# Kernel optimization log

Measured on AMD Instinct MI355X. Metric: run time of the kernel, lower is better.

The kernel has to match this reference:

```python
import jax, jax.numpy as jnp
import numpy as np

H = 512; W = 512; C = 32; B = 2; N = 120000; HEADS = 2; HD = C // HEADS; S = 9
INDEX_SHIFT = jnp.array([[0,0],[-1,0],[1,0],[0,1],[-1,1],[1,1],[0,-1],[-1,-1],[1,-1]], dtype=jnp.int32)


def setup_inputs() -> dict:
    key = jax.random.key(0)
    ks = jax.random.split(key, 20)
    bev_feats = jax.random.normal(ks[0], (B, N, C), jnp.float32)
    coors = []
    for b in range(B):
        perm = jax.random.permutation(ks[1 + b], H * W)[:N]
        coors.append(jnp.stack([perm // W, perm % W], axis=-1))
    bev_coors = jnp.stack(coors).astype(jnp.int32)
    s = 1.0 / np.sqrt(C)
    u = lambda k, shape, lim: jax.random.uniform(k, shape, jnp.float32, -lim, lim)
    return {
        'bev_feats': bev_feats,
        'bev_coors': bev_coors,
        'ln_w': jnp.ones((C,), jnp.float32),
        'ln_b': jnp.zeros((C,), jnp.float32),
        'wq': u(ks[3], (C, C), s), 'bq': u(ks[4], (C,), s),
        'wk': u(ks[5], (C, C), s), 'bk': u(ks[6], (C,), s),
        'wv': u(ks[7], (C, C), s), 'bv': u(ks[8], (C,), s),
        'pos_w': u(ks[9], (C, 2), 1.0 / np.sqrt(2.0)), 'pos_b': u(ks[10], (C,), 1.0 / np.sqrt(2.0)),
        'in_w': u(ks[11], (3 * C, C), s), 'in_b': jnp.zeros((3 * C,), jnp.float32),
        'out_w': u(ks[12], (C, C), s), 'out_b': jnp.zeros((C,), jnp.float32),
    }


def reference(bev_feats, bev_coors, ln_w, ln_b, wq, bq, wk, bk, wv, bv, pos_w, pos_b, in_w, in_b, out_w, out_b):
    def single(feats, coors):
        # LayerNorm (biased var, eps=1e-5)
        mu = feats.mean(-1, keepdims=True)
        var = feats.var(-1, keepdims=True)
        x = (feats - mu) / jnp.sqrt(var + 1e-5) * ln_w + ln_b
        # qkv 1x1 conv == linear
        q = x @ wq.T + bq
        k = x @ wk.T + bk
        v = x @ wv.T + bv
        # dense grid lookup: coord -> voxel index (-1 if empty)
        flat0 = coors[:, 0] * W + coors[:, 1]
        grid = jnp.full((H * W,), -1, jnp.int32).at[flat0].set(jnp.arange(N, dtype=jnp.int32))
        sc = coors[None] + INDEX_SHIFT[:, None]                      # [9,N,2]
        valid = (sc[..., 0] >= 0) & (sc[..., 0] < H) & (sc[..., 1] >= 0) & (sc[..., 1] < W)
        flat = jnp.clip(sc[..., 0], 0, H - 1) * W + jnp.clip(sc[..., 1], 0, W - 1)
        idx = jnp.where(valid, grid[flat], -1)                       # [9,N]
        pos = INDEX_SHIFT.astype(x.dtype) @ pos_w.T + pos_b          # [9,C]
        m = (idx >= 0)[..., None]
        tv = jnp.where(m, v[idx] + pos[:, None, :], 0.0)             # [9,N,C]
        tk = jnp.where(m, k[idx], 0.0)
        keyt = jnp.swapaxes(tk, 0, 1)                                # [N,9,C]
        valt = jnp.swapaxes(tv, 0, 1)
        # tiny MHA: query len 1, kv len 9, 2 heads (dropout inactive at eval)
        qp = q @ in_w[:C].T + in_b[:C]
        kp = keyt @ in_w[C:2 * C].T + in_b[C:2 * C]
        vp = valt @ in_w[2 * C:].T + in_b[2 * C:]
        qh = qp.reshape(N, HEADS, HD)
        kh = kp.reshape(N, S, HEADS, HD)
        vh = vp.reshape(N, S, HEADS, HD)
        attn = jax.nn.softmax(jnp.einsum('nhd,nshd->nhs', qh, kh) / np.sqrt(HD), axis=-1)
        o = jnp.einsum('nhs,nshd->nhd', attn, vh).reshape(N, C)
        o = o @ out_w.T + out_b
        # scatter to pseudo image [C,H,W]
        canvas = jnp.zeros((C, H * W), o.dtype).at[:, flat0].set(o.T)
        return canvas.reshape(C, H, W)
    return jax.vmap(single)(bev_feats, bev_coors)
```

## Files before the change

### kernel.cpp

```cpp
#include <hip/hip_runtime.h>
#include <hip/hip_fp16.h>
#include <cstdio>
#include <cstdint>

#define HH 512
#define WW 512
#define CC 32
#define BB 2
#define NN 120000
#define HWPIX (HH*WW)
#define NPTS (BB*NN)
#define NPIX (BB*HWPIX)
#define NBLK (NPIX/256)

__device__ __forceinline__ void h8_to_f8(float4 raw, float* o) {
    const __half2* h = (const __half2*)&raw;
    #pragma unroll
    for (int i = 0; i < 4; ++i) {
        float2 f = __half22float2(h[i]);
        o[2 * i] = f.x; o[2 * i + 1] = f.y;
    }
}

__global__ __launch_bounds__(256) void prep(const float* __restrict__ wq, const float* __restrict__ wk,
                          const float* __restrict__ wv, const float* __restrict__ in_w,
                          const float* __restrict__ out_w,
                          const float* __restrict__ bq, const float* __restrict__ bk,
                          const float* __restrict__ bv, const float* __restrict__ in_b,
                          const float* __restrict__ pos_w, const float* __restrict__ pos_b,
                          float* __restrict__ M, float* __restrict__ V, int* __restrict__ fmap_i) {
    int blk = blockIdx.x;
    if (blk < 16) {
        int tid = blk * 256 + threadIdx.x;
        int which = tid >> 10;
        int e = tid & 1023;
        int cp = e & 31;
        int j  = e >> 5;
        if (which < 3) {
            const float* w = (which == 0) ? wq : ((which == 1) ? wk : wv);
            const float* Wrow = in_w + (which * 32 + cp) * 32;
            float acc = 0.f;
            #pragma unroll
            for (int t = 0; t < 32; ++t) acc += Wrow[t] * w[t * 32 + j];
            M[which * 1024 + j * 32 + cp] = acc;
        } else {
            M[3 * 1024 + j * 32 + cp] = out_w[cp * 32 + j];
        }
    } else if (blk == 16) {
        int tid = threadIdx.x;
        if (tid < 32) {
            float a = 0.f, b = 0.f, c = 0.f;
            #pragma unroll
            for (int t = 0; t < 32; ++t) {
                a += in_w[tid * 32 + t] * bq[t];
                b += in_w[(32 + tid) * 32 + t] * bk[t];
                c += in_w[(64 + tid) * 32 + t] * bv[t];
            }
            V[tid]      = a + in_b[tid];
            V[32 + tid] = b;
            V[64 + tid] = c;
        } else if (tid < 128) {
            int grp = (tid - 32) >> 5;
            int cp  = tid & 31;
            float acc = 0.f;
            #pragma unroll
            for (int t = 0; t < 32; ++t) {
                float src = (grp == 0) ? pos_w[t * 2 + 0] : ((grp == 1) ? pos_w[t * 2 + 1] : pos_b[t]);
                acc += in_w[(64 + cp) * 32 + t] * src;
            }
            V[96 + grp * 32 + cp] = acc;
        }
    } else {
        int base = (blk - 17) * 2048 + threadIdx.x * 8;
        int4 z = {0, 0, 0, 0};
        *(int4*)(fmap_i + base)     = z;
        *(int4*)(fmap_i + base + 4) = z;
    }
}

__global__ __launch_bounds__(256) void stage1(const float* __restrict__ feats,
                                              const int* __restrict__ coors,
                                              const float* __restrict__ ln_w,
                                              const float* __restrict__ ln_b,
                                              const float* __restrict__ M,
                                              const float* __restrict__ V,
                                              __half* __restrict__ qh,
                                              __half* __restrict__ kvh,
                                              unsigned char* __restrict__ fmap) {
    int gp = blockIdx.x * 256 + threadIdx.x;
    if (gp >= NPTS) return;
    int b = (gp >= NN) ? 1 : 0;
    int2 yx = ((const int2*)coors)[gp];
    int pix = (b << 18) + (yx.x << 9) + yx.y;

    const float* fr = feats + ((size_t)gp << 5);
    float x[32];
    #pragma unroll
    for (int k = 0; k < 8; ++k) ((float4*)x)[k] = ((const float4*)fr)[k];

    float s1 = 0.f, s2 = 0.f;
    #pragma unroll
    for (int j = 0; j < 32; ++j) { s1 += x[j]; s2 += x[j] * x[j]; }
    float mu   = s1 * (1.f / 32.f);
    float var  = s2 * (1.f / 32.f) - mu * mu;
    float rstd = rsqrtf(var + 1e-5f);
    #pragma unroll
    for (int j = 0; j < 32; ++j) x[j] = (x[j] - mu) * rstd * ln_w[j] + ln_b[j];

    float acc[32];
    __half2 hbuf[16];

    #pragma unroll
    for (int c = 0; c < 32; ++c) acc[c] = V[c];
    #pragma unroll
    for (int j = 0; j < 32; ++j) {
        float xv = x[j];
        #pragma unroll
        for (int c = 0; c < 32; ++c) acc[c] += xv * M[j * 32 + c];
    }
    #pragma unroll
    for (int c = 0; c < 16; ++c) hbuf[c] = __floats2half2_rn(acc[2 * c], acc[2 * c + 1]);
    {
        float4* qd = (float4*)(qh + ((size_t)pix << 5));
        #pragma unroll
        for (int k = 0; k < 4; ++k) qd[k] = ((float4*)hbuf)[k];
    }

    __half2 kvbuf[32];

    #pragma unroll
    for (int c = 0; c < 32; ++c) acc[c] = V[32 + c];
    #pragma unroll
    for (int j = 0; j < 32; ++j) {
        float xv = x[j];
        #pragma unroll
        for (int c = 0; c < 32; ++c) acc[c] += xv * M[1024 + j * 32 + c];
    }
    #pragma unroll
    for (int c = 0; c < 16; ++c) kvbuf[c] = __floats2half2_rn(acc[2 * c], acc[2 * c + 1]);

    #pragma unroll
    for (int c = 0; c < 32; ++c) acc[c] = V[64 + c];
    #pragma unroll
    for (int j = 0; j < 32; ++j) {
        float xv = x[j];
        #pragma unroll
        for (int c = 0; c < 32; ++c) acc[c] += xv * M[2048 + j * 32 + c];
    }
    #pragma unroll
    for (int c = 0; c < 16; ++c) kvbuf[16 + c] = __floats2half2_rn(acc[2 * c], acc[2 * c + 1]);

    float4* kd = (float4*)(kvh + ((size_t)pix << 6));
    #pragma unroll
    for (int k = 0; k < 8; ++k) kd[k] = ((float4*)kvbuf)[k];

    fmap[pix] = 1;
}

__global__ __launch_bounds__(256) void stage23(const unsigned char* __restrict__ fmap,
                                               const __half* __restrict__ qh,
                                               const __half* __restrict__ kvh,
                                               const float* __restrict__ M,
                                               const float* __restrict__ V,
                                               const float* __restrict__ in_b,
                                               const float* __restrict__ out_b,
                                               float* __restrict__ out) {
    __shared__ __half2 lso[256 * 17];
    __shared__ int lsp[256];
    __shared__ int woff[4];

    int w = (blockIdx.x & 7) * 256 + (blockIdx.x >> 3);
    int tid = threadIdx.x;
    int pix = w * 256 + tid;

    bool occ = fmap[pix] != 0;
    unsigned long long mask = __ballot(occ);
    int lane = tid & 63, wvi = tid >> 6;
    if (lane == 0) woff[wvi] = __popcll(mask);
    __syncthreads();
    int pre = 0;
    for (int ww = 0; ww < wvi; ++ww) pre += woff[ww];
    int cnt = woff[0] + woff[1] + woff[2] + woff[3];
    int slot = -1;
    if (occ) {
        slot = pre + __popcll(mask & ((1ull << lane) - 1ull));
        lsp[slot] = tid;
    }
    __syncthreads();

    const int DYC[9] = {0,-1,1,0,-1,1,0,-1,1};
    const int DXC[9] = {0,0,0,1,1,1,-1,-1,-1};

    if (tid < cnt) {
        int pixl = w * 256 + lsp[tid];
        int b = pixl >> 18;
        int p = pixl & (HWPIX - 1);
        int y = p >> 9, x = p & 511;

        float qf[32];
        {
            const float4* q4 = (const float4*)(qh + ((size_t)pixl << 5));
            float4 r0 = q4[0], r1 = q4[1], r2 = q4[2], r3 = q4[3];
            h8_to_f8(r0, qf); h8_to_f8(r1, qf + 8); h8_to_f8(r2, qf + 16); h8_to_f8(r3, qf + 24);
        }

        int np[9];
        bool nv[9];
        #pragma unroll
        for (int s = 0; s < 9; ++s) {
            int sy = y + DYC[s], sx = x + DXC[s];
            bool inb = (sy >= 0) & (sy < HH) & (sx >= 0) & (sx < WW);
            int npx = (b << 18) + (sy << 9) + sx;
            np[s] = npx;
            nv[s] = inb ? (fmap[npx] != 0) : false;
        }

        float eb0 = 0.f, eb1 = 0.f;
        #pragma unroll
        for (int c = 0; c < 16; ++c) {
            eb0 += qf[c]      * in_b[32 + c];
            eb1 += qf[16 + c] * in_b[48 + c];
        }

        float lg0[9], lg1[9];
        #pragma unroll
        for (int s = 0; s < 9; ++s) {
            float d0 = eb0, d1 = eb1;
            if (nv[s]) {
                const float4* kp = (const float4*)(kvh + ((size_t)np[s] << 6));
                float kf[32];
                h8_to_f8(kp[0], kf);      h8_to_f8(kp[1], kf + 8);
                h8_to_f8(kp[2], kf + 16); h8_to_f8(kp[3], kf + 24);
                #pragma unroll
                for (int c = 0; c < 16; ++c) {
                    d0 += qf[c]      * kf[c];
                    d1 += qf[16 + c] * kf[16 + c];
                }
            }
            lg0[s] = d0 * 0.25f;
            lg1[s] = d1 * 0.25f;
        }
        float m0 = lg0[0], m1 = lg1[0];
        #pragma unroll
        for (int s = 1; s < 9; ++s) { m0 = fmaxf(m0, lg0[s]); m1 = fmaxf(m1, lg1[s]); }
        float l0 = 0.f, l1 = 0.f;
        #pragma unroll
        for (int s = 0; s < 9; ++s) {
            lg0[s] = __expf(lg0[s] - m0); l0 += lg0[s];
            lg1[s] = __expf(lg1[s] - m1); l1 += lg1[s];
        }

        float o[32];
        #pragma unroll
        for (int c = 0; c < 32; ++c) o[c] = 0.f;
        float wdy0 = 0.f, wdx0 = 0.f, woc0 = 0.f;
        float wdy1 = 0.f, wdx1 = 0.f, woc1 = 0.f;
        #pragma unroll
        for (int s = 0; s < 9; ++s) {
            if (nv[s]) {
                float w0 = lg0[s], w1 = lg1[s];
                const float4* vp = (const float4*)(kvh + ((size_t)np[s] << 6)) + 4;
                float vf[32];
                h8_to_f8(vp[0], vf);      h8_to_f8(vp[1], vf + 8);
                h8_to_f8(vp[2], vf + 16); h8_to_f8(vp[3], vf + 24);
                #pragma unroll
                for (int c = 0; c < 16; ++c) {
                    o[c]      += w0 * vf[c];
                    o[16 + c] += w1 * vf[16 + c];
                }
                wdy0 += w0 * (float)DYC[s]; wdx0 += w0 * (float)DXC[s]; woc0 += w0;
                wdy1 += w1 * (float)DYC[s]; wdx1 += w1 * (float)DXC[s]; woc1 += w1;
            }
        }
        float rl0 = 1.f / l0, rl1 = 1.f / l1;
        #pragma unroll
        for (int c = 0; c < 16; ++c) {
            o[c]      = (o[c]      + wdy0 * V[96 + c]      + wdx0 * V[128 + c]      + woc0 * V[160 + c])      * rl0 + in_b[64 + c];
            o[16 + c] = (o[16 + c] + wdy1 * V[96 + 16 + c] + wdx1 * V[128 + 16 + c] + woc1 * V[160 + 16 + c]) * rl1 + in_b[80 + c];
        }

        float acc[32];
        #pragma unroll
        for (int c = 0; c < 32; ++c) acc[c] = out_b[c];
        #pragma unroll
        for (int j = 0; j < 32; ++j) {
            float vj = o[j];
            #pragma unroll
            for (int c = 0; c < 32; ++c) acc[c] += vj * M[3072 + j * 32 + c];
        }

        __half2* lrow = lso + tid * 17;
        #pragma unroll
        for (int c = 0; c < 16; ++c) lrow[c] = __floats2half2_rn(acc[2 * c], acc[2 * c + 1]);
    }
    __syncthreads();

    int b = pix >> 18;
    int p = pix & (HWPIX - 1);
    float* outb = out + (size_t)b * CC * HWPIX + p;
    if (occ) {
        const __half2* lrow = lso + slot * 17;
        #pragma unroll
        for (int c2 = 0; c2 < 16; ++c2) {
            float2 f = __half22float2(lrow[c2]);
            outb[(2 * c2) * HWPIX]     = f.x;
            outb[(2 * c2 + 1) * HWPIX] = f.y;
        }
    } else {
        #pragma unroll
        for (int cc = 0; cc < 32; ++cc) outb[cc * HWPIX] = 0.f;
    }
}

extern "C" void kernel_launch(void* const* d_in, const int* in_sizes, int n_in,
                              void* d_out, int out_size, void* d_ws, size_t ws_size,
                              hipStream_t stream) {
    const float* feats = (const float*)d_in[0];
    const int*   coors = (const int*)d_in[1];
    const float* ln_w  = (const float*)d_in[2];
    const float* ln_b  = (const float*)d_in[3];
    const float* wq    = (const float*)d_in[4];
    const float* bq    = (const float*)d_in[5];
    const float* wk    = (const float*)d_in[6];
    const float* bk    = (const float*)d_in[7];
    const float* wv    = (const float*)d_in[8];
    const float* bv    = (const float*)d_in[9];
    const float* pos_w = (const float*)d_in[10];
    const float* pos_b = (const float*)d_in[11];
    const float* in_w  = (const float*)d_in[12];
    const float* in_b  = (const float*)d_in[13];
    const float* out_w = (const float*)d_in[14];
    const float* out_b = (const float*)d_in[15];

    float*  M    = (float*)d_ws;
    float*  V    = M + 4096;
    __half* qh   = (__half*)(V + 192);
    __half* kvh  = qh + (size_t)NPIX * 32;
    unsigned char* fmap = (unsigned char*)(kvh + (size_t)NPIX * 64);
    size_t need = (4096 + 192) * 4 + (size_t)NPIX * 96 * 2 + (size_t)NPIX;
    if (ws_size < need) {
        fprintf(stderr, "kernel_launch: ws too small: %zu < %zu\n", ws_size, need);
        return;
    }

    prep<<<81, 256, 0, stream>>>(wq, wk, wv, in_w, out_w, bq, bk, bv, in_b, pos_w, pos_b,
                                 M, V, (int*)fmap);
    stage1<<<(NPTS + 255) / 256, 256, 0, stream>>>(feats, coors, ln_w, ln_b, M, V, qh, kvh, fmap);
    stage23<<<NBLK, 256, 0, stream>>>(fmap, qh, kvh, M, V, in_b, out_b, (float*)d_out);
}
```

Measured before the change: 193.3 us.

## Split per-pixel attention across two threads, one per head

Each occupied pixel is now processed by two adjacent threads, each handling one attention head's key/value gathers, softmax and weighted sum. Head outputs are exchanged via a lane shuffle before the output projection, and each thread writes half of the output channels to shared memory. This raises lane utilization of the compacted work and lowers per-thread register pressure. In exchange, the output projection is computed redundantly in both threads.

```diff
diff --git a/kernel.cpp b/kernel.cpp
--- a/kernel.cpp
+++ b/kernel.cpp
@@ -165,7 +165,7 @@
                                                const float* __restrict__ in_b,
                                                const float* __restrict__ out_b,
                                                float* __restrict__ out) {
-    __shared__ __half2 lso[256 * 17];
+    __shared__ __half2 lso[256 * 18];
     __shared__ int lsp[256];
     __shared__ int woff[4];
 
@@ -191,17 +191,18 @@
     const int DYC[9] = {0,-1,1,0,-1,1,0,-1,1};
     const int DXC[9] = {0,0,0,1,1,1,-1,-1,-1};
 
-    if (tid < cnt) {
-        int pixl = w * 256 + lsp[tid];
+    for (int task = tid; task < 2 * cnt; task += 256) {
+        int i = task >> 1, h = task & 1;
+        int pixl = w * 256 + lsp[i];
         int b = pixl >> 18;
         int p = pixl & (HWPIX - 1);
         int y = p >> 9, x = p & 511;
 
-        float qf[32];
+        float qf[16];
         {
-            const float4* q4 = (const float4*)(qh + ((size_t)pixl << 5));
-            float4 r0 = q4[0], r1 = q4[1], r2 = q4[2], r3 = q4[3];
-            h8_to_f8(r0, qf); h8_to_f8(r1, qf + 8); h8_to_f8(r2, qf + 16); h8_to_f8(r3, qf + 24);
+            const float4* q4 = (const float4*)(qh + ((size_t)pixl << 5) + (h << 4));
+            float4 r0 = q4[0], r1 = q4[1];
+            h8_to_f8(r0, qf); h8_to_f8(r1, qf + 8);
         }
 
         int np[9];
@@ -215,68 +216,68 @@
             nv[s] = inb ? (fmap[npx] != 0) : false;
         }
 
-        float eb0 = 0.f, eb1 = 0.f;
-        #pragma unroll
-        for (int c = 0; c < 16; ++c) {
-            eb0 += qf[c]      * in_b[32 + c];
-            eb1 += qf[16 + c] * in_b[48 + c];
-        }
-
-        float lg0[9], lg1[9];
+        float eb = 0.f;
+        {
+            const float* ib = in_b + 32 + (h << 4);
+            #pragma unroll
+            for (int c = 0; c < 16; ++c) eb += qf[c] * ib[c];
+        }
+
+        float lg[9];
         #pragma unroll
         for (int s = 0; s < 9; ++s) {
-            float d0 = eb0, d1 = eb1;
+            float d = eb;
             if (nv[s]) {
-                const float4* kp = (const float4*)(kvh + ((size_t)np[s] << 6));
-                float kf[32];
-                h8_to_f8(kp[0], kf);      h8_to_f8(kp[1], kf + 8);
-                h8_to_f8(kp[2], kf + 16); h8_to_f8(kp[3], kf + 24);
+                const float4* kp = (const float4*)(kvh + ((size_t)np[s] << 6) + (h << 4));
+                float kf[16];
+                float4 k0 = kp[0], k1 = kp[1];
+                h8_to_f8(k0, kf); h8_to_f8(k1, kf + 8);
                 #pragma unroll
-                for (int c = 0; c < 16; ++c) {
-                    d0 += qf[c]      * kf[c];
-                    d1 += qf[16 + c] * kf[16 + c];
-                }
+                for (int c = 0; c < 16; ++c) d += qf[c] * kf[c];
             }
-            lg0[s] = d0 * 0.25f;
-            lg1[s] = d1 * 0.25f;
-        }
-        float m0 = lg0[0], m1 = lg1[0];
-        #pragma unroll
-        for (int s = 1; s < 9; ++s) { m0 = fmaxf(m0, lg0[s]); m1 = fmaxf(m1, lg1[s]); }
-        float l0 = 0.f, l1 = 0.f;
-        #pragma unroll
-        for (int s = 0; s < 9; ++s) {
-            lg0[s] = __expf(lg0[s] - m0); l0 += lg0[s];
-            lg1[s] = __expf(lg1[s] - m1); l1 += lg1[s];
-        }
-
-        float o[32];
-        #pragma unroll
-        for (int c = 0; c < 32; ++c) o[c] = 0.f;
-        float wdy0 = 0.f, wdx0 = 0.f, woc0 = 0.f;
-        float wdy1 = 0.f, wdx1 = 0.f, woc1 = 0.f;
+            lg[s] = d * 0.25f;
+        }
+        float m = lg[0];
+        #pragma unroll
+        for (int s = 1; s < 9; ++s) m = fmaxf(m, lg[s]);
+        float l = 0.f;
+        #pragma unroll
+        for (int s = 0; s < 9; ++s) { lg[s] = __expf(lg[s] - m); l += lg[s]; }
+
+        float o16[16];
+        #pragma unroll
+        for (int c = 0; c < 16; ++c) o16[c] = 0.f;
+        float wdy = 0.f, wdx = 0.f, woc = 0.f;
         #pragma unroll
         for (int s = 0; s < 9; ++s) {
             if (nv[s]) {
-                float w0 = lg0[s], w1 = lg1[s];
-                const float4* vp = (const float4*)(kvh + ((size_t)np[s] << 6)) + 4;
-                float vf[32];
-                h8_to_f8(vp[0], vf);      h8_to_f8(vp[1], vf + 8);
-                h8_to_f8(vp[2], vf + 16); h8_to_f8(vp[3], vf + 24);
+                float wgt = lg[s];
+                const float4* vp = (const float4*)(kvh + ((size_t)np[s] << 6) + 32 + (h << 4));
+                float vf[16];
+                float4 v0 = vp[0], v1 = vp[1];
+                h8_to_f8(v0, vf); h8_to_f8(v1, vf + 8);
                 #pragma unroll
-                for (int c = 0; c < 16; ++c) {
-                    o[c]      += w0 * vf[c];
-                    o[16 + c] += w1 * vf[16 + c];
-                }
-                wdy0 += w0 * (float)DYC[s]; wdx0 += w0 * (float)DXC[s]; woc0 += w0;
-                wdy1 += w1 * (float)DYC[s]; wdx1 += w1 * (float)DXC[s]; woc1 += w1;
+                for (int c = 0; c < 16; ++c) o16[c] += wgt * vf[c];
+                wdy += wgt * (float)DYC[s]; wdx += wgt * (float)DXC[s]; woc += wgt;
             }
         }
-        float rl0 = 1.f / l0, rl1 = 1.f / l1;
-        #pragma unroll
-        for (int c = 0; c < 16; ++c) {
-            o[c]      = (o[c]      + wdy0 * V[96 + c]      + wdx0 * V[128 + c]      + woc0 * V[160 + c])      * rl0 + in_b[64 + c];
-            o[16 + c] = (o[16 + c] + wdy1 * V[96 + 16 + c] + wdx1 * V[128 + 16 + c] + woc1 * V[160 + 16 + c]) * rl1 + in_b[80 + c];
+        float rl = 1.f / l;
+        {
+            const float* PY = V + 96 + (h << 4);
+            const float* PX = V + 128 + (h << 4);
+            const float* PB = V + 160 + (h << 4);
+            const float* B3 = in_b + 64 + (h << 4);
+            #pragma unroll
+            for (int c = 0; c < 16; ++c)
+                o16[c] = (o16[c] + wdy * PY[c] + wdx * PX[c] + woc * PB[c]) * rl + B3[c];
+        }
+
+        float of[32];
+        #pragma unroll
+        for (int j = 0; j < 16; ++j) {
+            float po = __shfl_xor(o16[j], 1, 64);
+            of[j]      = h ? po : o16[j];
+            of[16 + j] = h ? o16[j] : po;
         }
 
         float acc[32];
@@ -284,14 +285,17 @@
         for (int c = 0; c < 32; ++c) acc[c] = out_b[c];
         #pragma unroll
         for (int j = 0; j < 32; ++j) {
-            float vj = o[j];
+            float vj = of[j];
             #pragma unroll
             for (int c = 0; c < 32; ++c) acc[c] += vj * M[3072 + j * 32 + c];
         }
 
-        __half2* lrow = lso + tid * 17;
-        #pragma unroll
-        for (int c = 0; c < 16; ++c) lrow[c] = __floats2half2_rn(acc[2 * c], acc[2 * c + 1]);
+        __half2* lrow = lso + i * 18 + (h << 3);
+        #pragma unroll
+        for (int c = 0; c < 8; ++c) {
+            int cc = (h << 4) + 2 * c;
+            lrow[c] = __floats2half2_rn(acc[cc], acc[cc + 1]);
+        }
     }
     __syncthreads();
 
@@ -299,7 +303,7 @@
     int p = pix & (HWPIX - 1);
     float* outb = out + (size_t)b * CC * HWPIX + p;
     if (occ) {
-        const __half2* lrow = lso + slot * 17;
+        const __half2* lrow = lso + slot * 18;
         #pragma unroll
         for (int c2 = 0; c2 < 16; ++c2) {
             float2 f = __half22float2(lrow[c2]);
```

Result: slower. 387.4 us (+100.3%).
